# Performance work log

Hardware: AMD Instinct MI355X
Metric: run time of the kernel (lower is better)

The kernel has to match this reference:

```python
import jax, jax.numpy as jnp
import numpy as np

H_FEATS = 256

def setup_inputs() -> dict:
    key = jax.random.key(0)
    k1, k2, k3, k4, k5, k6, k7 = jax.random.split(key, 7)
    N, E, D = 100000, 500000, H_FEATS
    h = jax.random.normal(k1, (N, D), dtype=jnp.float32)
    src = jax.random.randint(k2, (E,), 0, N)
    dst = jax.random.randint(k3, (E,), 0, N)
    # Linear params (PyTorch default init: U(-1/sqrt(fan_in), 1/sqrt(fan_in)))
    b1_bound = 1.0 / np.sqrt(2 * D)
    b2_bound = 1.0 / np.sqrt(D)
    W1 = jax.random.uniform(k4, (2 * D, D), jnp.float32, -b1_bound, b1_bound)
    b1 = jax.random.uniform(k5, (D,), jnp.float32, -b1_bound, b1_bound)
    W2 = jax.random.uniform(k6, (D, 1), jnp.float32, -b2_bound, b2_bound)
    b2 = jax.random.uniform(k7, (1,), jnp.float32, -b2_bound, b2_bound)
    return {"h": h, "src": src, "dst": dst, "W1": W1, "b1": b1, "W2": W2, "b2": b2}

def reference(h, src, dst, W1, b1, W2, b2):
    # Gather per-edge source/destination node features and concat: [E, 2D]
    he = jnp.concatenate([h[src], h[dst]], axis=1)
    # Linear -> ReLU -> (dropout is identity in eval) -> Linear -> Sigmoid
    hid = jax.nn.relu(he @ W1 + b1)          # [E, D]
    score = jax.nn.sigmoid((hid @ W2 + b2).squeeze(1))  # [E]
    return score
```

## Files before the change

### kernel.cpp

```cpp
#include <hip/hip_runtime.h>
#include <math.h>


typedef __attribute__((ext_vector_type(8))) short short8;
typedef __attribute__((ext_vector_type(2))) float floatx2;
typedef __attribute__((ext_vector_type(4))) float floatx4;
typedef __attribute__((ext_vector_type(16))) float floatx16;

#define D_FEAT 256
#define EPW 8

__device__ __forceinline__ float bf2f(unsigned short u) {
    union { unsigned u32; float f; } v; v.u32 = ((unsigned)u) << 16; return v.f;
}
__device__ __forceinline__ float lo16(unsigned u) {
    union { unsigned u32; float f; } v; v.u32 = u << 16; return v.f;
}
__device__ __forceinline__ float hi16(unsigned u) {
    union { unsigned u32; float f; } v; v.u32 = u & 0xffff0000u; return v.f;
}
__device__ __forceinline__ unsigned short f2bf(float f) {
    union { float f; unsigned u32; } v; v.f = f;
    unsigned x = v.u32;
    return (unsigned short)((x + 0x7fffu + ((x >> 16) & 1u)) >> 16);
}
__device__ __forceinline__ float sigmoid_safe(float r) {
    r = fminf(fmaxf(r, -30.f), 30.f);
    return 1.f / (1.f + expf(-r));
}
__device__ __forceinline__ unsigned pack4_fp8(float a, float b, float c, float d) {
    int w = __builtin_amdgcn_cvt_pk_fp8_f32(a, b, 0, false);
    w = __builtin_amdgcn_cvt_pk_fp8_f32(c, d, w, true);
    return (unsigned)w;
}

__global__ __launch_bounds__(256) void probe_dtype(const unsigned short* __restrict__ h,
                                                   int* __restrict__ flag) {
    __shared__ int cnt[256];
    const int t = threadIdx.x;
    int c = 0;
    #pragma unroll
    for (int i = 0; i < 8; ++i) {
        unsigned e = (h[t * 8 + i] >> 7) & 0xFF;
        c += (e >= 100 && e <= 140) ? 1 : 0;
    }
    cnt[t] = c;
    __syncthreads();
    if (t == 0) {
        int s = 0;
        for (int i = 0; i < 256; ++i) s += cnt[i];
        flag[0] = (s >= 1843) ? 1 : 0;
    }
}

template <int MODE>
__global__ __launch_bounds__(256) void build_wt_t(const void* __restrict__ W1v,
                                                  unsigned short* __restrict__ Wt,
                                                  const int* __restrict__ flag) {
    if (flag[0] != MODE) return;
    int j = blockIdx.x, k = threadIdx.x;
    size_t idx = (j < 256) ? ((size_t)k * 256 + j) : ((size_t)(k + 256) * 256 + (j - 256));
    unsigned short v;
    if constexpr (MODE == 1) v = ((const unsigned short*)W1v)[idx];
    else                     v = f2bf(((const float*)W1v)[idx]);
    Wt[(size_t)j * 256 + k] = v;
}

template <int MODE>
__global__ __launch_bounds__(512, 2) void gemm_pq_t(const void* __restrict__ hv,
                                                    const unsigned short* __restrict__ Wt,
                                                    unsigned char* __restrict__ PQ8,
                                                    int N, const int* __restrict__ flag) {
    if (flag[0] != MODE) return;
    __shared__ unsigned short As[2][64][256];

    const int tid  = threadIdx.x;
    const int lane = tid & 63;
    const int wid  = tid >> 6;
    const int l32  = lane & 31;
    const int q2   = lane >> 5;

    short8 breg0[16], breg1[16];
    {
        const char* bp0 = (const char*)Wt + (size_t)(wid * 64 + l32) * 512 + q2 * 16;
        const char* bp1 = bp0 + 32 * 512;
        #pragma unroll
        for (int ks = 0; ks < 16; ++ks) {
            breg0[ks] = *(const short8*)(bp0 + ks * 32);
            breg1[ks] = *(const short8*)(bp1 + ks * 32);
        }
    }

    const int ar = tid >> 3;
    const unsigned ac = (unsigned)(tid & 7) * 64;
    const unsigned aswz = ((unsigned)ar & 31) << 4;

    short8  pref[4];
    floatx4 pf[8];
    auto load_a = [&](int ms) {
        const int gm = ms * 64 + ar;
        if constexpr (MODE == 1) {
            #pragma unroll
            for (int j = 0; j < 4; ++j) {
                short8 v = {};
                if (gm < N)
                    v = *(const short8*)((const char*)hv + (size_t)gm * 512 + ac + j * 16);
                pref[j] = v;
            }
        } else {
            #pragma unroll
            for (int j = 0; j < 4; ++j) {
                floatx4 f0 = {}, f1 = {};
                if (gm < N) {
                    const float* p = (const float*)hv + (size_t)gm * 256 + (ac + j * 16) / 2;
                    f0 = *(const floatx4*)p;
                    f1 = *(const floatx4*)(p + 4);
                }
                pf[2 * j]     = f0;
                pf[2 * j + 1] = f1;
            }
        }
    };
    auto write_a = [&](int p) {
        char* adst = (char*)&As[p][0][0] + (unsigned)ar * 512;
        #pragma unroll
        for (int j = 0; j < 4; ++j) {
            short8 v;
            if constexpr (MODE == 1) {
                v = pref[j];
            } else {
                floatx4 f0 = pf[2 * j], f1 = pf[2 * j + 1];
                v[0] = (short)f2bf(f0.x); v[1] = (short)f2bf(f0.y);
                v[2] = (short)f2bf(f0.z); v[3] = (short)f2bf(f0.w);
                v[4] = (short)f2bf(f1.x); v[5] = (short)f2bf(f1.y);
                v[6] = (short)f2bf(f1.z); v[7] = (short)f2bf(f1.w);
            }
            *(short8*)(adst + ((ac + j * 16) ^ aswz)) = v;
        }
    };

    const int NT = (N + 63) >> 6;
    const int GM = gridDim.x;
    const int bid = blockIdx.x;

    load_a(bid);
    write_a(0);
    if (bid + GM < NT) load_a(bid + GM);
    __syncthreads();

    int p = 0;
    for (int ms = bid; ms < NT; ms += GM) {
        write_a(p ^ 1);
        if (ms + 2 * GM < NT) load_a(ms + 2 * GM);

        floatx16 acc[2][2] = {};
        const char* abase = (const char*)&As[p][0][0];
        #pragma unroll
        for (int ks = 0; ks < 16; ++ks) {
            const unsigned cb = ((unsigned)(ks * 32 + q2 * 16)) ^ ((unsigned)l32 << 4);
            short8 a0 = *(const short8*)(abase + (unsigned)l32 * 512 + cb);
            short8 a1 = *(const short8*)(abase + (unsigned)(32 + l32) * 512 + cb);
            acc[0][0] = __builtin_amdgcn_mfma_f32_32x32x16_bf16(breg0[ks], a0, acc[0][0], 0, 0, 0);
            acc[1][0] = __builtin_amdgcn_mfma_f32_32x32x16_bf16(breg0[ks], a1, acc[1][0], 0, 0, 0);
            acc[0][1] = __builtin_amdgcn_mfma_f32_32x32x16_bf16(breg1[ks], a0, acc[0][1], 0, 0, 0);
            acc[1][1] = __builtin_amdgcn_mfma_f32_32x32x16_bf16(breg1[ks], a1, acc[1][1], 0, 0, 0);
        }

        const int m_base = ms * 64;
        #pragma unroll
        for (int mi = 0; mi < 2; ++mi) {
            int m = m_base + mi * 32 + l32;
            if (m < N) {
                #pragma unroll
                for (int nb = 0; nb < 2; ++nb) {
                    int cbase = wid * 64 + nb * 32 + 4 * q2;
                    #pragma unroll
                    for (int g = 0; g < 4; ++g) {
                        unsigned w = pack4_fp8(acc[mi][nb][4 * g + 0], acc[mi][nb][4 * g + 1],
                                               acc[mi][nb][4 * g + 2], acc[mi][nb][4 * g + 3]);
                        *(unsigned*)(PQ8 + (size_t)m * 512 + cbase + 8 * g) = w;
                    }
                }
            }
        }

        __syncthreads();
        p ^= 1;
    }
}

template <int MODE>
__global__ __launch_bounds__(256) void edge_score_t(const unsigned char* __restrict__ PQ8,
                                                    const int* __restrict__ src,
                                                    const int* __restrict__ dst,
                                                    const void* __restrict__ b1v,
                                                    const void* __restrict__ W2v,
                                                    const void* __restrict__ b2v,
                                                    void* __restrict__ outv,
                                                    int E, const int* __restrict__ flag) {
    if (flag[0] != MODE) return;
    const int wave = threadIdx.x >> 6;
    const int lane = threadIdx.x & 63;
    const int e0 = (blockIdx.x * 4 + wave) * EPW;
    if (e0 >= E) return;
    const int l32 = lane & 31;
    const int* __restrict__ idxp = (lane >= 32) ? dst : src;

    float bf[8], wf[8];
    if constexpr (MODE == 1) {
        const uint4 bvr = *(const uint4*)((const unsigned short*)b1v + l32 * 8);
        const uint4 wvr = *(const uint4*)((const unsigned short*)W2v + l32 * 8);
        bf[0] = lo16(bvr.x); bf[1] = hi16(bvr.x); bf[2] = lo16(bvr.y); bf[3] = hi16(bvr.y);
        bf[4] = lo16(bvr.z); bf[5] = hi16(bvr.z); bf[6] = lo16(bvr.w); bf[7] = hi16(bvr.w);
        wf[0] = lo16(wvr.x); wf[1] = hi16(wvr.x); wf[2] = lo16(wvr.y); wf[3] = hi16(wvr.y);
        wf[4] = lo16(wvr.z); wf[5] = hi16(wvr.z); wf[6] = lo16(wvr.w); wf[7] = hi16(wvr.w);
    } else {
        const float* bp = (const float*)b1v + l32 * 8;
        const float* wp = (const float*)W2v + l32 * 8;
        #pragma unroll
        for (int t = 0; t < 8; ++t) { bf[t] = bp[t]; wf[t] = wp[t]; }
    }

    int node[EPW];
    #pragma unroll
    for (int i = 0; i < EPW; ++i) {
        int e = e0 + i; if (e >= E) e = E - 1;
        node[i] = idxp[e];
    }
    uint2 raw[EPW];
    #pragma unroll
    for (int i = 0; i < EPW; ++i)
        raw[i] = *(const uint2*)(PQ8 + (size_t)node[i] * 512 + lane * 8);

    float res[EPW];
    #pragma unroll
    for (int i = 0; i < EPW; ++i) {
        uint2 o;
        o.x = (unsigned)__shfl_xor((int)raw[i].x, 32);
        o.y = (unsigned)__shfl_xor((int)raw[i].y, 32);
        floatx2 p01 = __builtin_amdgcn_cvt_pk_f32_fp8((int)raw[i].x, false);
        floatx2 p23 = __builtin_amdgcn_cvt_pk_f32_fp8((int)raw[i].x, true);
        floatx2 p45 = __builtin_amdgcn_cvt_pk_f32_fp8((int)raw[i].y, false);
        floatx2 p67 = __builtin_amdgcn_cvt_pk_f32_fp8((int)raw[i].y, true);
        floatx2 q01 = __builtin_amdgcn_cvt_pk_f32_fp8((int)o.x, false);
        floatx2 q23 = __builtin_amdgcn_cvt_pk_f32_fp8((int)o.x, true);
        floatx2 q45 = __builtin_amdgcn_cvt_pk_f32_fp8((int)o.y, false);
        floatx2 q67 = __builtin_amdgcn_cvt_pk_f32_fp8((int)o.y, true);
        float v0 = fmaxf(p01.x + q01.x + bf[0], 0.f);
        float v1 = fmaxf(p01.y + q01.y + bf[1], 0.f);
        float v2 = fmaxf(p23.x + q23.x + bf[2], 0.f);
        float v3 = fmaxf(p23.y + q23.y + bf[3], 0.f);
        float v4 = fmaxf(p45.x + q45.x + bf[4], 0.f);
        float v5 = fmaxf(p45.y + q45.y + bf[5], 0.f);
        float v6 = fmaxf(p67.x + q67.x + bf[6], 0.f);
        float v7 = fmaxf(p67.y + q67.y + bf[7], 0.f);
        float sum = v0 * wf[0] + v1 * wf[1] + v2 * wf[2] + v3 * wf[3]
                  + v4 * wf[4] + v5 * wf[5] + v6 * wf[6] + v7 * wf[7];
        #pragma unroll
        for (int off = 1; off <= 16; off <<= 1)
            sum += __shfl_xor(sum, off);
        res[i] = sum;
    }

    if (lane == 0) {
        float bias2;
        if constexpr (MODE == 1) bias2 = bf2f(((const unsigned short*)b2v)[0]);
        else                     bias2 = ((const float*)b2v)[0];
        if constexpr (MODE == 1) {
            union { short8 v; unsigned short u[8]; } r;
            #pragma unroll
            for (int i = 0; i < EPW; ++i)
                r.u[i] = f2bf(sigmoid_safe(res[i] + bias2));
            unsigned short* outp = (unsigned short*)outv;
            if (e0 + EPW <= E) *(short8*)(outp + e0) = r.v;
            else for (int i = 0; i < EPW && e0 + i < E; ++i) outp[e0 + i] = r.u[i];
        } else {
            float* outp = (float*)outv;
            for (int i = 0; i < EPW && e0 + i < E; ++i)
                outp[e0 + i] = sigmoid_safe(res[i] + bias2);
        }
    }
}

template <int MODE>
__global__ __launch_bounds__(256) void edge_fused_t(const void* __restrict__ hv,
                                                    const int* __restrict__ src,
                                                    const int* __restrict__ dst,
                                                    const void* __restrict__ W1v,
                                                    const void* __restrict__ b1v,
                                                    const void* __restrict__ W2v,
                                                    const void* __restrict__ b2v,
                                                    void* __restrict__ outv,
                                                    int E, const int* __restrict__ flag) {
    if (flag && flag[0] != MODE) return;
    __shared__ float he[512];
    __shared__ float wsum[4];
    const int e = blockIdx.x;
    if (e >= E) return;
    const int t = threadIdx.x;
    const int s = src[e];
    const int d = dst[e];

    if constexpr (MODE == 1) {
        he[t]       = bf2f(((const unsigned short*)hv)[(size_t)s * 256 + t]);
        he[256 + t] = bf2f(((const unsigned short*)hv)[(size_t)d * 256 + t]);
    } else {
        he[t]       = ((const float*)hv)[(size_t)s * 256 + t];
        he[256 + t] = ((const float*)hv)[(size_t)d * 256 + t];
    }
    __syncthreads();

    float acc;
    if constexpr (MODE == 1) acc = bf2f(((const unsigned short*)b1v)[t]);
    else                     acc = ((const float*)b1v)[t];

    #pragma unroll 8
    for (int k = 0; k < 512; ++k) {
        float w;
        if constexpr (MODE == 1) w = bf2f(((const unsigned short*)W1v)[(size_t)k * 256 + t]);
        else                     w = ((const float*)W1v)[(size_t)k * 256 + t];
        acc += he[k] * w;
    }

    float w2;
    if constexpr (MODE == 1) w2 = bf2f(((const unsigned short*)W2v)[t]);
    else                     w2 = ((const float*)W2v)[t];
    acc = fmaxf(acc, 0.f) * w2;

    #pragma unroll
    for (int off = 32; off > 0; off >>= 1)
        acc += __shfl_xor(acc, off);
    if ((t & 63) == 0) wsum[t >> 6] = acc;
    __syncthreads();

    if (t == 0) {
        float bias2;
        if constexpr (MODE == 1) bias2 = bf2f(((const unsigned short*)b2v)[0]);
        else                     bias2 = ((const float*)b2v)[0];
        float r = sigmoid_safe(wsum[0] + wsum[1] + wsum[2] + wsum[3] + bias2);
        if constexpr (MODE == 1) ((unsigned short*)outv)[e] = f2bf(r);
        else                     ((float*)outv)[e] = r;
    }
}

extern "C" void kernel_launch(void* const* d_in, const int* in_sizes, int n_in,
                              void* d_out, int out_size, void* d_ws, size_t ws_size,
                              hipStream_t stream) {
    const void* h  = d_in[0];
    const int* src = (const int*)d_in[1];
    const int* dst = (const int*)d_in[2];
    const void* W1 = d_in[3];
    const void* b1 = d_in[4];
    const void* W2 = d_in[5];
    const void* b2 = d_in[6];

    const int N = in_sizes[0] / D_FEAT;
    const int E = in_sizes[1];

    const size_t FLAG_BYTES = 256;
    const size_t wt_bytes  = (size_t)512 * D_FEAT * sizeof(unsigned short);
    const size_t pq_bytes  = (size_t)N * 512;
    const size_t need = FLAG_BYTES + wt_bytes + pq_bytes;

    int* flag = (int*)d_ws;
    unsigned short* Wt = (unsigned short*)((char*)d_ws + FLAG_BYTES);
    unsigned char*  PQ8 = (unsigned char*)((char*)d_ws + FLAG_BYTES + wt_bytes);

    if (ws_size >= need) {
        probe_dtype<<<1, 256, 0, stream>>>((const unsigned short*)h, flag);

        build_wt_t<1><<<512, 256, 0, stream>>>(W1, Wt, flag);
        build_wt_t<0><<<512, 256, 0, stream>>>(W1, Wt, flag);

        gemm_pq_t<1><<<256, 512, 0, stream>>>(h, Wt, PQ8, N, flag);
        gemm_pq_t<0><<<256, 512, 0, stream>>>(h, Wt, PQ8, N, flag);

        int egrid = (E + 4 * EPW - 1) / (4 * EPW);
        edge_score_t<1><<<egrid, 256, 0, stream>>>(PQ8, src, dst, b1, W2, b2, d_out, E, flag);
        edge_score_t<0><<<egrid, 256, 0, stream>>>(PQ8, src, dst, b1, W2, b2, d_out, E, flag);
    } else if (ws_size >= FLAG_BYTES) {
        probe_dtype<<<1, 256, 0, stream>>>((const unsigned short*)h, flag);
        edge_fused_t<1><<<E, 256, 0, stream>>>(h, src, dst, W1, b1, W2, b2, d_out, E, flag);
        edge_fused_t<0><<<E, 256, 0, stream>>>(h, src, dst, W1, b1, W2, b2, d_out, E, flag);
    } else {
        edge_fused_t<1><<<E, 256, 0, stream>>>(h, src, dst, W1, b1, W2, b2, d_out, E, nullptr);
    }
}
```

Baseline: 284.6 us.

## Stage FP8 GEMM output through LDS for coalesced 16-byte global stores

After: 286.2 us. No clear change (+0.6%).

```diff
diff --git a/kernel.cpp b/kernel.cpp
--- a/kernel.cpp
+++ b/kernel.cpp
@@ -72,7 +72,8 @@
                                                     unsigned char* __restrict__ PQ8,
                                                     int N, const int* __restrict__ flag) {
     if (flag[0] != MODE) return;
-    __shared__ unsigned short As[2][64][256];
+    __shared__ unsigned short As[64][256];
+    __shared__ unsigned char  Scr[64][512];
 
     const int tid  = threadIdx.x;
     const int lane = tid & 63;
@@ -121,8 +122,8 @@
             }
         }
     };
-    auto write_a = [&](int p) {
-        char* adst = (char*)&As[p][0][0] + (unsigned)ar * 512;
+    auto write_a = [&]() {
+        char* adst = (char*)&As[0][0] + (unsigned)ar * 512;
         #pragma unroll
         for (int j = 0; j < 4; ++j) {
             short8 v;
@@ -144,17 +145,15 @@
     const int bid = blockIdx.x;
 
     load_a(bid);
-    write_a(0);
-    if (bid + GM < NT) load_a(bid + GM);
-    __syncthreads();
-
-    int p = 0;
+
     for (int ms = bid; ms < NT; ms += GM) {
-        write_a(p ^ 1);
-        if (ms + 2 * GM < NT) load_a(ms + 2 * GM);
+        write_a();
+        __syncthreads();
+
+        if (ms + GM < NT) load_a(ms + GM);
 
         floatx16 acc[2][2] = {};
-        const char* abase = (const char*)&As[p][0][0];
+        const char* abase = (const char*)&As[0][0];
         #pragma unroll
         for (int ks = 0; ks < 16; ++ks) {
             const unsigned cb = ((unsigned)(ks * 32 + q2 * 16)) ^ ((unsigned)l32 << 4);
@@ -166,26 +165,38 @@
             acc[1][1] = __builtin_amdgcn_mfma_f32_32x32x16_bf16(breg1[ks], a1, acc[1][1], 0, 0, 0);
         }
 
-        const int m_base = ms * 64;
-        #pragma unroll
-        for (int mi = 0; mi < 2; ++mi) {
-            int m = m_base + mi * 32 + l32;
-            if (m < N) {
+        {
+            unsigned char* scr = (unsigned char*)&Scr[0][0];
+            #pragma unroll
+            for (int mi = 0; mi < 2; ++mi) {
+                const unsigned row = (unsigned)(mi * 32 + l32);
+                const unsigned rs = (row & 31) << 4;
                 #pragma unroll
                 for (int nb = 0; nb < 2; ++nb) {
-                    int cbase = wid * 64 + nb * 32 + 4 * q2;
+                    const unsigned nbase = (unsigned)(wid * 64 + nb * 32 + 4 * q2);
                     #pragma unroll
                     for (int g = 0; g < 4; ++g) {
                         unsigned w = pack4_fp8(acc[mi][nb][4 * g + 0], acc[mi][nb][4 * g + 1],
                                                acc[mi][nb][4 * g + 2], acc[mi][nb][4 * g + 3]);
-                        *(unsigned*)(PQ8 + (size_t)m * 512 + cbase + 8 * g) = w;
+                        *(unsigned*)(scr + ((row * 512 + nbase + 8 * g) ^ rs)) = w;
                     }
                 }
             }
         }
-
         __syncthreads();
-        p ^= 1;
+
+        {
+            const unsigned char* scr = (const unsigned char*)&Scr[0][0];
+            const int gm = ms * 64 + ar;
+            if (gm < N) {
+                #pragma unroll
+                for (int j = 0; j < 4; ++j) {
+                    const unsigned col = ac + j * 16;
+                    uint4 v = *(const uint4*)(scr + (((unsigned)ar * 512 + col) ^ aswz));
+                    *(uint4*)(PQ8 + (size_t)gm * 512 + col) = v;
+                }
+            }
+        }
     }
 }
 
```
